# Kernel tuning notes

Hardware: AMD Instinct MI355X
Metric: run time of the kernel (lower is better)

The kernel has to match this reference:

```python
import jax, jax.numpy as jnp
import numpy as np

NUM_HEADS = 12


def setup_inputs() -> dict:
    key = jax.random.key(0)
    ks = jax.random.split(key, 6)
    B, T, D = 512, 128, 768  # batch, seq (<= CONTEXT_LENGTH=128), d_model
    d_in, d_out = D, D
    s_in = 1.0 / np.sqrt(d_in)
    s_out = 1.0 / np.sqrt(d_out)
    return {
        "x": jax.random.normal(ks[0], (B, T, d_in), dtype=jnp.float32),
        "Wq": jax.random.uniform(ks[1], (d_in, d_out), jnp.float32, -s_in, s_in),
        "Wk": jax.random.uniform(ks[2], (d_in, d_out), jnp.float32, -s_in, s_in),
        "Wv": jax.random.uniform(ks[3], (d_in, d_out), jnp.float32, -s_in, s_in),
        "Wo": jax.random.uniform(ks[4], (d_out, d_out), jnp.float32, -s_out, s_out),
        "bo": jax.random.uniform(ks[5], (d_out,), jnp.float32, -s_out, s_out),
    }


def reference(x, Wq, Wk, Wv, Wo, bo):
    B, T, _ = x.shape
    H = NUM_HEADS
    hd = Wq.shape[1] // H
    # projections -> [b, h, t, hd]
    q = jnp.einsum("btd,de->bte", x, Wq).reshape(B, T, H, hd).transpose(0, 2, 1, 3)
    k = jnp.einsum("btd,de->bte", x, Wk).reshape(B, T, H, hd).transpose(0, 2, 1, 3)
    v = jnp.einsum("btd,de->bte", x, Wv).reshape(B, T, H, hd).transpose(0, 2, 1, 3)
    scores = jnp.einsum("bhqd,bhkd->bhqk", q, k)
    causal = jnp.tril(jnp.ones((T, T), dtype=bool))  # True = keep
    scores = jnp.where(causal, scores, -jnp.inf)
    attn = jax.nn.softmax(scores / jnp.sqrt(jnp.float32(hd)), axis=-1)
    # dropout is identity in eval mode
    ctx = jnp.einsum("bhqk,bhkd->bhqd", attn, v)
    ctx = ctx.transpose(0, 2, 1, 3).reshape(B, T, H * hd)
    return jnp.einsum("btd,de->bte", ctx, Wo) + bo
```

## Files before the change

kernel.cpp:

```cpp
#include <hip/hip_runtime.h>
#include <hip/hip_bf16.h>
#include <cstdint>
#include <math.h>


typedef __bf16 bf16;
typedef __bf16 bf16x8 __attribute__((ext_vector_type(8)));
typedef float f32x4 __attribute__((ext_vector_type(4)));

#define MFMA16(a, b, c) __builtin_amdgcn_mfma_f32_16x16x32_bf16((a), (b), (c), 0, 0, 0)

#define GLD_LDS16(gp, lp)                                                       \
  __builtin_amdgcn_global_load_lds(                                             \
      (const __attribute__((address_space(1))) void*)(gp),                      \
      (__attribute__((address_space(3))) void*)(lp), 16, 0, 0)

__global__ __launch_bounds__(256) void cast_x_bf16(const float* __restrict__ in,
                                                   bf16* __restrict__ out, int n) {
  int i = (blockIdx.x * 256 + threadIdx.x) * 4;
  if (i < n) {
    float4 v = *(const float4*)(in + i);
    bf16 o[4] = {(bf16)v.x, (bf16)v.y, (bf16)v.z, (bf16)v.w};
    *(uint2*)(out + i) = *(const uint2*)o;
  }
}

__global__ __launch_bounds__(256) void transpose_cast_w(const float* __restrict__ W,
                                                        bf16* __restrict__ Out) {
  __shared__ float t[32][33];
  int bx = blockIdx.x * 32;
  int by = blockIdx.y * 32;
  int tx = threadIdx.x, ty = threadIdx.y;
  for (int i = 0; i < 32; i += 8)
    t[ty + i][tx] = W[(size_t)(bx + ty + i) * 768 + by + tx];
  __syncthreads();
  for (int i = 0; i < 32; i += 8)
    Out[(size_t)(by + ty + i) * 768 + bx + tx] = (bf16)t[tx][ty + i];
}

template <bool OUT_F32>
__global__ __launch_bounds__(512, 2) void gemm256(
    const bf16* __restrict__ A, int lda, const bf16* __restrict__ Bt, int ldb,
    void* __restrict__ Cout, int ldc, const float* __restrict__ bias, int K,
    int ntn) {
  __shared__ bf16 smem[2 * 32768];

  const int tid = threadIdx.x;
  const int lane = tid & 63;
  const int w = tid >> 6;

  const int nwg = gridDim.x;
  const int wg = (blockIdx.x & 7) * (nwg >> 3) + (blockIdx.x >> 3);
  const int m0 = (wg / ntn) * 256;
  const int n0 = (wg % ntn) * 256;

  const int r0 = tid >> 2;
  const int c0 = ((((tid & 3) * 16) ^ (((tid >> 3) & 3) << 4)) >> 1);
  const bf16* As0 = A + (size_t)(m0 + r0) * lda + c0;
  const bf16* As1 = As0 + (size_t)128 * lda;
  const bf16* Bs0 = Bt + (size_t)(n0 + r0) * ldb + c0;
  const bf16* Bs1 = Bs0 + (size_t)128 * ldb;

  const int lm = lane & 15;
  const int kqs = ((lane >> 4) * 8) ^ (((lm >> 1) & 3) << 3);
  const int wm = (w & 1) * 128;
  const int wn = (w >> 1) * 64;
  const bf16* pA = smem + (wm + lm) * 32 + kqs;
  const bf16* pB = smem + 16384 + (wn + lm) * 32 + kqs;

  f32x4 acc[8][4];
#pragma unroll
  for (int i = 0; i < 8; ++i)
#pragma unroll
    for (int j = 0; j < 4; ++j) acc[i][j] = (f32x4){0.f, 0.f, 0.f, 0.f};

  bf16x8 af[4], bfr[4];

  const int NT = K >> 6;
  const int NH = NT >> 1;

  auto SA = [&](int t, int kh) {
    const int ko = t * 64 + kh * 32;
    const int lo = (t & 1) * 32768 + kh * 8192;
    GLD_LDS16(As0 + ko, smem + lo + w * 512);
    GLD_LDS16(As1 + ko, smem + lo + 4096 + w * 512);
  };
  auto SB = [&](int t, int kh) {
    const int ko = t * 64 + kh * 32;
    const int lo = (t & 1) * 32768 + 16384 + kh * 8192;
    GLD_LDS16(Bs0 + ko, smem + lo + w * 512);
    GLD_LDS16(Bs1 + ko, smem + lo + 4096 + w * 512);
  };
  auto RD = [&](int buf, int kh, int h, bool lb) {
    const bf16* a = pA + buf * 32768 + kh * 8192 + h * 2048;
#pragma unroll
    for (int j = 0; j < 4; ++j) af[j] = *(const bf16x8*)(a + j * 512);
    if (lb) {
      const bf16* b = pB + buf * 32768 + kh * 8192;
#pragma unroll
      for (int j = 0; j < 4; ++j) bfr[j] = *(const bf16x8*)(b + j * 512);
    }
  };
  auto BARMID = [&](int vm) {
    if (vm == 6) asm volatile("s_waitcnt vmcnt(6)" ::: "memory");
    else if (vm == 0) asm volatile("s_waitcnt vmcnt(0)" ::: "memory");
    __builtin_amdgcn_s_barrier();
    asm volatile("s_waitcnt lgkmcnt(0)" ::: "memory");
    __builtin_amdgcn_sched_barrier(0);
  };
  auto BAREND = [&]() {
    __builtin_amdgcn_s_barrier();
    __builtin_amdgcn_sched_barrier(0);
  };
  auto MM = [&](int h) {
    __builtin_amdgcn_s_setprio(1);
#pragma unroll
    for (int j = 0; j < 4; ++j)
#pragma unroll
      for (int n = 0; n < 4; ++n)
        acc[h * 4 + j][n] = MFMA16(af[j], bfr[n], acc[h * 4 + j][n]);
    __builtin_amdgcn_s_setprio(0);
  };

  SB(0, 0); SA(0, 0); SB(0, 1); SA(0, 1);
  asm volatile("s_waitcnt vmcnt(4)" ::: "memory");
  SB(1, 0); SA(1, 0); SB(1, 1);
  asm volatile("s_waitcnt vmcnt(6)" ::: "memory");
  __builtin_amdgcn_s_barrier();
  __builtin_amdgcn_sched_barrier(0);

  for (int i = 0; i < NH - 1; ++i) {
    const int t1 = 2 * i + 1, t2 = 2 * i + 2, t3 = 2 * i + 3;
    RD(0, 0, 0, true);  SA(t1, 1); BARMID(-1); MM(0); BAREND();
    RD(0, 0, 1, false); SB(t2, 0); BARMID(-1); MM(1); BAREND();
    RD(0, 1, 0, true);  SA(t2, 0); BARMID(-1); MM(0); BAREND();
    RD(0, 1, 1, false); SB(t2, 1); BARMID(6);  MM(1); BAREND();
    RD(1, 0, 0, true);  SA(t2, 1); BARMID(-1); MM(0); BAREND();
    RD(1, 0, 1, false); SB(t3, 0); BARMID(-1); MM(1); BAREND();
    RD(1, 1, 0, true);  SA(t3, 0); BARMID(-1); MM(0); BAREND();
    RD(1, 1, 1, false); SB(t3, 1); BARMID(6);  MM(1); BAREND();
  }
  RD(0, 0, 0, true);  SA(NT - 1, 1); BARMID(-1); MM(0); BAREND();
  RD(0, 0, 1, false);                BARMID(-1); MM(1); BAREND();
  RD(0, 1, 0, true);                 BARMID(-1); MM(0); BAREND();
  RD(0, 1, 1, false);                BARMID(0);  MM(1); BAREND();
  RD(1, 0, 0, true);                 BARMID(-1); MM(0); BAREND();
  RD(1, 0, 1, false);                BARMID(-1); MM(1); BAREND();
  RD(1, 1, 0, true);                 BARMID(-1); MM(0); BAREND();
  RD(1, 1, 1, false);                BARMID(-1); MM(1); BAREND();

  __syncthreads();

  const int lr = (lane >> 4) * 4;
  if constexpr (!OUT_F32) {
    const unsigned exw = (unsigned)(lane >> 4) << 5;
#pragma unroll
    for (int mi = 0; mi < 8; ++mi)
#pragma unroll
      for (int ni = 0; ni < 4; ++ni) {
        const int colb = (wn + ni * 16 + lm) * 2;
#pragma unroll
        for (int r = 0; r < 4; ++r) {
          const unsigned ad = (unsigned)(wm + mi * 16 + lr + r) * 512 + colb;
          *(bf16*)((char*)smem + (ad ^ exw)) = (bf16)acc[mi][ni][r];
        }
      }
    __syncthreads();
    const unsigned exr = (unsigned)((tid >> 7) & 3) << 5;
#pragma unroll
    for (int s = 0; s < 16; ++s) {
      const int e = s * 4096 + tid * 8;
      const int row = e >> 8, col = e & 255;
      uint4 v = *(const uint4*)((char*)smem + (((unsigned)row * 512 + col * 2) ^ exr));
      *(uint4*)((bf16*)Cout + (size_t)(m0 + row) * ldc + n0 + col) = v;
    }
  } else {
    const unsigned exw = (unsigned)(lane >> 4) << 6;
#pragma unroll
    for (int h = 0; h < 2; ++h) {
      __syncthreads();
      if ((w & 1) == h) {
#pragma unroll
        for (int mi = 0; mi < 8; ++mi)
#pragma unroll
          for (int ni = 0; ni < 4; ++ni) {
            const int colb = (wn + ni * 16 + lm) * 4;
#pragma unroll
            for (int r = 0; r < 4; ++r) {
              const unsigned ad = (unsigned)(mi * 16 + lr + r) * 1024 + colb;
              *(float*)((char*)smem + (ad ^ exw)) = acc[mi][ni][r];
            }
          }
      }
      __syncthreads();
#pragma unroll
      for (int s = 0; s < 16; ++s) {
        const int row = s * 8 + w;
        const int col = (lane & 63) * 4;
        const unsigned xr = (unsigned)((row >> 2) & 3) << 6;
        float4 v = *(const float4*)((char*)smem + (((unsigned)row * 1024 + col * 4) ^ xr));
        float4 bb = *(const float4*)(bias + n0 + col);
        v.x += bb.x; v.y += bb.y; v.z += bb.z; v.w += bb.w;
        *(float4*)((float*)Cout + (size_t)(m0 + h * 128 + row) * ldc + n0 + col) = v;
      }
    }
  }
}

__global__ __launch_bounds__(256) void attn_kernel(const bf16* __restrict__ qkv,
                                                   bf16* __restrict__ ctx) {
  constexpr int LDQ = 2304;
  constexpr int SQS = 72;
  constexpr int SPS = 136;
  __shared__ bf16 smem[27136];
  bf16* sQ = smem;
  bf16* sK = smem + 128 * SQS;
  bf16* sVt = smem + 2 * 128 * SQS;
  bf16* sP = smem;

  const int bh = (blockIdx.x & 7) * 768 + (blockIdx.x >> 3);
  const int b = bh / 12, h = bh % 12;
  const bf16* Qg = qkv + (size_t)b * 128 * LDQ + h * 64;
  const bf16* Kg = Qg + 768;
  const bf16* Vg = Qg + 1536;

  const int tid = threadIdx.x;
  {
    int row = tid >> 1, half = tid & 1;
    const uint4* qsrc = (const uint4*)(Qg + (size_t)row * LDQ + half * 32);
    const uint4* ksrc = (const uint4*)(Kg + (size_t)row * LDQ + half * 32);
    const uint4* vsrc = (const uint4*)(Vg + (size_t)row * LDQ + half * 32);
    uint4* qdst = (uint4*)(sQ + row * SQS + half * 32);
    uint4* kdst = (uint4*)(sK + row * SQS + half * 32);
    uint4 vt[4];
    for (int i = 0; i < 4; ++i) {
      qdst[i] = qsrc[i];
      kdst[i] = ksrc[i];
      vt[i] = vsrc[i];
    }
    const bf16* tp = (const bf16*)vt;
    for (int d = 0; d < 32; ++d) sVt[(half * 32 + d) * SPS + row] = tp[d];
  }
  __syncthreads();

  const int lane = tid & 63;
  const int w = tid >> 6;
  const int lm = lane & 15;
  const int kq = (lane >> 4) * 8;
  const int lr = (lane >> 4) * 4;

  f32x4 sacc[2][8];
  for (int i = 0; i < 2; ++i)
    for (int j = 0; j < 8; ++j) sacc[i][j] = (f32x4){0.f, 0.f, 0.f, 0.f};
  for (int kk = 0; kk < 64; kk += 32) {
    bf16x8 aq[2], bk[8];
    for (int mi = 0; mi < 2; ++mi)
      aq[mi] = *(const bf16x8*)(sQ + (w * 32 + mi * 16 + lm) * SQS + kk + kq);
    for (int ni = 0; ni < 8; ++ni)
      bk[ni] = *(const bf16x8*)(sK + (ni * 16 + lm) * SQS + kk + kq);
    for (int mi = 0; mi < 2; ++mi)
      for (int ni = 0; ni < 8; ++ni)
        sacc[mi][ni] = MFMA16(aq[mi], bk[ni], sacc[mi][ni]);
  }

  float inv[2][4];
  for (int mi = 0; mi < 2; ++mi) {
    for (int r = 0; r < 4; ++r) {
      int row = w * 32 + mi * 16 + lr + r;
      float vals[8];
      float mx = -INFINITY;
      for (int ni = 0; ni < 8; ++ni) {
        int col = ni * 16 + lm;
        float v = sacc[mi][ni][r] * 0.125f;
        if (col > row) v = -INFINITY;
        vals[ni] = v;
        mx = fmaxf(mx, v);
      }
      for (int off = 1; off < 16; off <<= 1) mx = fmaxf(mx, __shfl_xor(mx, off, 64));
      float sum = 0.f;
      for (int ni = 0; ni < 8; ++ni) {
        float p = __expf(vals[ni] - mx);
        vals[ni] = p;
        sum += p;
      }
      for (int off = 1; off < 16; off <<= 1) sum += __shfl_xor(sum, off, 64);
      inv[mi][r] = 1.f / sum;
      for (int ni = 0; ni < 8; ++ni) sacc[mi][ni][r] = vals[ni];
    }
  }
  __syncthreads();

  for (int mi = 0; mi < 2; ++mi)
    for (int ni = 0; ni < 8; ++ni)
      for (int r = 0; r < 4; ++r) {
        int row = w * 32 + mi * 16 + lr + r;
        int col = ni * 16 + lm;
        sP[row * SPS + col] = (bf16)sacc[mi][ni][r];
      }
  __syncthreads();

  f32x4 oacc[2][4];
  for (int i = 0; i < 2; ++i)
    for (int j = 0; j < 4; ++j) oacc[i][j] = (f32x4){0.f, 0.f, 0.f, 0.f};
  for (int kk = 0; kk < 128; kk += 32) {
    bf16x8 ap[2], bv[4];
    for (int mi = 0; mi < 2; ++mi)
      ap[mi] = *(const bf16x8*)(sP + (w * 32 + mi * 16 + lm) * SPS + kk + kq);
    for (int ci = 0; ci < 4; ++ci)
      bv[ci] = *(const bf16x8*)(sVt + (ci * 16 + lm) * SPS + kk + kq);
    for (int mi = 0; mi < 2; ++mi)
      for (int ci = 0; ci < 4; ++ci)
        oacc[mi][ci] = MFMA16(ap[mi], bv[ci], oacc[mi][ci]);
  }

  bf16* Cg = ctx + (size_t)b * 128 * LDQ + h * 64;
  for (int mi = 0; mi < 2; ++mi)
    for (int ci = 0; ci < 4; ++ci)
      for (int r = 0; r < 4; ++r) {
        int row = w * 32 + mi * 16 + lr + r;
        int col = ci * 16 + lm;
        Cg[(size_t)row * LDQ + col] = (bf16)(oacc[mi][ci][r] * inv[mi][r]);
      }
}

extern "C" void kernel_launch(void* const* d_in, const int* in_sizes, int n_in,
                              void* d_out, int out_size, void* d_ws, size_t ws_size,
                              hipStream_t stream) {
  const float* x = (const float*)d_in[0];
  const float* Wq = (const float*)d_in[1];
  const float* Wk = (const float*)d_in[2];
  const float* Wv = (const float*)d_in[3];
  const float* Wo = (const float*)d_in[4];
  const float* bo = (const float*)d_in[5];
  float* out = (float*)d_out;

  constexpr int M = 512 * 128;
  constexpr int D = 768;
  constexpr size_t XB_BYTES = (size_t)M * D * 2;
  constexpr size_t WQKV_BYTES = (size_t)3 * D * D * 2;
  constexpr size_t WOT_BYTES = (size_t)D * D * 2;

  char* ws = (char*)d_ws;
  bf16* xb = (bf16*)ws;
  bf16* wqkv = (bf16*)(ws + XB_BYTES);
  bf16* wot = (bf16*)(ws + XB_BYTES + WQKV_BYTES);
  bf16* qkv = (bf16*)(ws + XB_BYTES + WQKV_BYTES + WOT_BYTES);

  cast_x_bf16<<<(M * D) / 1024, 256, 0, stream>>>(x, xb, M * D);
  dim3 tb(32, 8);
  transpose_cast_w<<<dim3(24, 24), tb, 0, stream>>>(Wq, wqkv);
  transpose_cast_w<<<dim3(24, 24), tb, 0, stream>>>(Wk, wqkv + 768 * 768);
  transpose_cast_w<<<dim3(24, 24), tb, 0, stream>>>(Wv, wqkv + 2 * 768 * 768);
  transpose_cast_w<<<dim3(24, 24), tb, 0, stream>>>(Wo, wot);
  gemm256<false><<<dim3(2304), 512, 0, stream>>>(xb, 768, wqkv, 768, qkv, 2304,
                                                 nullptr, 768, 9);
  attn_kernel<<<512 * 12, 256, 0, stream>>>(qkv, qkv);
  gemm256<true><<<dim3(768), 512, 0, stream>>>(qkv, 2304, wot, 768, out, 768,
                                               bo, 768, 3);
}
```

Baseline: 788.8 us.

## Load Q fragments directly to registers, shrink attention LDS, merge GEMM barriers

In the attention kernel, Q is no longer staged through shared memory: each wave loads its MFMA A-fragments straight from global memory into registers. This shrinks the LDS footprint and adds a launch bound targeting 3 blocks per CU to raise occupancy. In the projection GEMM main loop, the trailing barrier after each MFMA phase is removed, so each phase has one barrier instead of two. Dropping that barrier risks LDS overwrite races unless the double-buffer schedule already guarantees the data has been consumed.

```diff
diff --git a/kernel.cpp b/kernel.cpp
--- a/kernel.cpp
+++ b/kernel.cpp
@@ -101,15 +101,12 @@
       for (int j = 0; j < 4; ++j) bfr[j] = *(const bf16x8*)(b + j * 512);
     }
   };
-  auto BARMID = [&](int vm) {
+  auto BAR = [&](int vm) {
+    __builtin_amdgcn_sched_barrier(0);
     if (vm == 6) asm volatile("s_waitcnt vmcnt(6)" ::: "memory");
     else if (vm == 0) asm volatile("s_waitcnt vmcnt(0)" ::: "memory");
     __builtin_amdgcn_s_barrier();
     asm volatile("s_waitcnt lgkmcnt(0)" ::: "memory");
-    __builtin_amdgcn_sched_barrier(0);
-  };
-  auto BAREND = [&]() {
-    __builtin_amdgcn_s_barrier();
     __builtin_amdgcn_sched_barrier(0);
   };
   auto MM = [&](int h) {
@@ -131,23 +128,23 @@
 
   for (int i = 0; i < NH - 1; ++i) {
     const int t1 = 2 * i + 1, t2 = 2 * i + 2, t3 = 2 * i + 3;
-    RD(0, 0, 0, true);  SA(t1, 1); BARMID(-1); MM(0); BAREND();
-    RD(0, 0, 1, false); SB(t2, 0); BARMID(-1); MM(1); BAREND();
-    RD(0, 1, 0, true);  SA(t2, 0); BARMID(-1); MM(0); BAREND();
-    RD(0, 1, 1, false); SB(t2, 1); BARMID(6);  MM(1); BAREND();
-    RD(1, 0, 0, true);  SA(t2, 1); BARMID(-1); MM(0); BAREND();
-    RD(1, 0, 1, false); SB(t3, 0); BARMID(-1); MM(1); BAREND();
-    RD(1, 1, 0, true);  SA(t3, 0); BARMID(-1); MM(0); BAREND();
-    RD(1, 1, 1, false); SB(t3, 1); BARMID(6);  MM(1); BAREND();
-  }
-  RD(0, 0, 0, true);  SA(NT - 1, 1); BARMID(-1); MM(0); BAREND();
-  RD(0, 0, 1, false);                BARMID(-1); MM(1); BAREND();
-  RD(0, 1, 0, true);                 BARMID(-1); MM(0); BAREND();
-  RD(0, 1, 1, false);                BARMID(0);  MM(1); BAREND();
-  RD(1, 0, 0, true);                 BARMID(-1); MM(0); BAREND();
-  RD(1, 0, 1, false);                BARMID(-1); MM(1); BAREND();
-  RD(1, 1, 0, true);                 BARMID(-1); MM(0); BAREND();
-  RD(1, 1, 1, false);                BARMID(-1); MM(1); BAREND();
+    RD(0, 0, 0, true);  SA(t1, 1); BAR(-1); MM(0);
+    RD(0, 0, 1, false); SB(t2, 0); BAR(-1); MM(1);
+    RD(0, 1, 0, true);  SA(t2, 0); BAR(-1); MM(0);
+    RD(0, 1, 1, false); SB(t2, 1); BAR(6);  MM(1);
+    RD(1, 0, 0, true);  SA(t2, 1); BAR(-1); MM(0);
+    RD(1, 0, 1, false); SB(t3, 0); BAR(-1); MM(1);
+    RD(1, 1, 0, true);  SA(t3, 0); BAR(-1); MM(0);
+    RD(1, 1, 1, false); SB(t3, 1); BAR(6);  MM(1);
+  }
+  RD(0, 0, 0, true);  SA(NT - 1, 1); BAR(-1); MM(0);
+  RD(0, 0, 1, false);                BAR(-1); MM(1);
+  RD(0, 1, 0, true);                 BAR(-1); MM(0);
+  RD(0, 1, 1, false);                BAR(0);  MM(1);
+  RD(1, 0, 0, true);                 BAR(-1); MM(0);
+  RD(1, 0, 1, false);                BAR(-1); MM(1);
+  RD(1, 1, 0, true);                 BAR(-1); MM(0);
+  RD(1, 1, 1, false);                BAR(-1); MM(1);
 
   __syncthreads();
 
@@ -207,16 +204,15 @@
   }
 }
 
-__global__ __launch_bounds__(256) void attn_kernel(const bf16* __restrict__ qkv,
-                                                   bf16* __restrict__ ctx) {
+__global__ __launch_bounds__(256, 3) void attn_kernel(const bf16* __restrict__ qkv,
+                                                      bf16* __restrict__ ctx) {
   constexpr int LDQ = 2304;
-  constexpr int SQS = 72;
+  constexpr int SKS = 72;
   constexpr int SPS = 136;
-  __shared__ bf16 smem[27136];
-  bf16* sQ = smem;
-  bf16* sK = smem + 128 * SQS;
-  bf16* sVt = smem + 2 * 128 * SQS;
+  __shared__ bf16 smem[26112];
+  bf16* sK = smem;
   bf16* sP = smem;
+  bf16* sVt = smem + 17408;
 
   const int bh = (blockIdx.x & 7) * 768 + (blockIdx.x >> 3);
   const int b = bh / 12, h = bh % 12;
@@ -225,42 +221,45 @@
   const bf16* Vg = Qg + 1536;
 
   const int tid = threadIdx.x;
-  {
-    int row = tid >> 1, half = tid & 1;
-    const uint4* qsrc = (const uint4*)(Qg + (size_t)row * LDQ + half * 32);
-    const uint4* ksrc = (const uint4*)(Kg + (size_t)row * LDQ + half * 32);
-    const uint4* vsrc = (const uint4*)(Vg + (size_t)row * LDQ + half * 32);
-    uint4* qdst = (uint4*)(sQ + row * SQS + half * 32);
-    uint4* kdst = (uint4*)(sK + row * SQS + half * 32);
-    uint4 vt[4];
-    for (int i = 0; i < 4; ++i) {
-      qdst[i] = qsrc[i];
-      kdst[i] = ksrc[i];
-      vt[i] = vsrc[i];
-    }
-    const bf16* tp = (const bf16*)vt;
-    for (int d = 0; d < 32; ++d) sVt[(half * 32 + d) * SPS + row] = tp[d];
-  }
-  __syncthreads();
-
   const int lane = tid & 63;
   const int w = tid >> 6;
   const int lm = lane & 15;
   const int kq = (lane >> 4) * 8;
   const int lr = (lane >> 4) * 4;
 
+  bf16x8 aq[2][2];
+#pragma unroll
+  for (int mi = 0; mi < 2; ++mi)
+#pragma unroll
+    for (int kk2 = 0; kk2 < 2; ++kk2)
+      aq[mi][kk2] = *(const bf16x8*)(Qg + (size_t)(w * 32 + mi * 16 + lm) * LDQ +
+                                     kk2 * 32 + kq);
+
+  {
+    int row = tid >> 1, half = tid & 1;
+    const uint4* ksrc = (const uint4*)(Kg + (size_t)row * LDQ + half * 32);
+    const uint4* vsrc = (const uint4*)(Vg + (size_t)row * LDQ + half * 32);
+    uint4* kdst = (uint4*)(sK + row * SKS + half * 32);
+    uint4 vt[4];
+    for (int i = 0; i < 4; ++i) {
+      kdst[i] = ksrc[i];
+      vt[i] = vsrc[i];
+    }
+    const bf16* tp = (const bf16*)vt;
+    for (int d = 0; d < 32; ++d) sVt[(half * 32 + d) * SPS + row] = tp[d];
+  }
+  __syncthreads();
+
   f32x4 sacc[2][8];
   for (int i = 0; i < 2; ++i)
     for (int j = 0; j < 8; ++j) sacc[i][j] = (f32x4){0.f, 0.f, 0.f, 0.f};
-  for (int kk = 0; kk < 64; kk += 32) {
-    bf16x8 aq[2], bk[8];
-    for (int mi = 0; mi < 2; ++mi)
-      aq[mi] = *(const bf16x8*)(sQ + (w * 32 + mi * 16 + lm) * SQS + kk + kq);
+  for (int kk2 = 0; kk2 < 2; ++kk2) {
+    bf16x8 bk[8];
     for (int ni = 0; ni < 8; ++ni)
-      bk[ni] = *(const bf16x8*)(sK + (ni * 16 + lm) * SQS + kk + kq);
+      bk[ni] = *(const bf16x8*)(sK + (ni * 16 + lm) * SKS + kk2 * 32 + kq);
     for (int mi = 0; mi < 2; ++mi)
       for (int ni = 0; ni < 8; ++ni)
-        sacc[mi][ni] = MFMA16(aq[mi], bk[ni], sacc[mi][ni]);
+        sacc[mi][ni] = MFMA16(aq[mi][kk2], bk[ni], sacc[mi][ni]);
   }
 
   float inv[2][4];
```

Result: faster. 767.0 us (-2.8%).
